# Optimization experiments

Hardware: AMD Instinct MI355X
Metric: run time of the kernel (lower is better)

The kernel has to match this reference:

```python
import jax, jax.numpy as jnp
import numpy as np

B_SZ, L_SEQ, ENC_IN = 8, 1024, 32
D_MODEL, D_INNER, D_STATE, D_CONV, DT_RANK = 256, 512, 16, 4, 16
N_LAYERS, D_FF, C_OUT = 2, 1024, 1


def setup_inputs() -> dict:
    key = jax.random.key(0)
    ks = jax.random.split(key, 16)
    s = 0.02
    inp = {}
    inp["x"] = jax.random.normal(ks[0], (B_SZ, L_SEQ, ENC_IN), jnp.float32)
    inp["in_w"] = jax.random.normal(ks[1], (D_MODEL, ENC_IN), jnp.float32) * s
    inp["in_b"] = jnp.zeros((D_MODEL,), jnp.float32)
    inp["in_proj_w"] = jax.random.normal(ks[2], (N_LAYERS, 2 * D_INNER, D_MODEL), jnp.float32) * s
    inp["conv_w"] = jax.random.normal(ks[3], (N_LAYERS, D_INNER, D_CONV), jnp.float32) * 0.1
    inp["conv_b"] = jnp.zeros((N_LAYERS, D_INNER), jnp.float32)
    inp["x_proj_w"] = jax.random.normal(ks[4], (N_LAYERS, DT_RANK + 2 * D_STATE, D_INNER), jnp.float32) * s
    inp["dt_w"] = jax.random.normal(ks[5], (N_LAYERS, D_INNER, DT_RANK), jnp.float32) * (DT_RANK ** -0.5)
    dt = jax.random.uniform(ks[6], (N_LAYERS, D_INNER), jnp.float32, 1e-3, 0.1)
    inp["dt_b"] = dt + jnp.log(-jnp.expm1(-dt))  # inverse softplus
    inp["A_log"] = jnp.tile(jnp.log(jnp.arange(1, D_STATE + 1, dtype=jnp.float32)), (N_LAYERS, D_INNER, 1))
    inp["D_skip"] = jnp.ones((N_LAYERS, D_INNER), jnp.float32)
    inp["out_proj_w"] = jax.random.normal(ks[7], (N_LAYERS, D_MODEL, D_INNER), jnp.float32) * s
    inp["p1_w"] = jax.random.normal(ks[8], (D_FF, D_MODEL), jnp.float32) * s
    inp["p1_b"] = jnp.zeros((D_FF,), jnp.float32)
    inp["p2_w"] = jax.random.normal(ks[9], (C_OUT, D_FF), jnp.float32) * s
    inp["p2_b"] = jnp.zeros((C_OUT,), jnp.float32)
    return inp


def causal_dw_conv(x, w, b):
    # x: [b, l, d], w: [d, k] depthwise, left-pad for causality
    xc = jax.lax.conv_general_dilated(
        x.transpose(0, 2, 1), w[:, None, :], (1,), [(D_CONV - 1, 0)],
        feature_group_count=D_INNER, dimension_numbers=("NCH", "OIH", "NCH"))
    return (xc + b[None, :, None]).transpose(0, 2, 1)


def selective_scan(u, dt, A, Bm, Cm):
    # u, dt: [b, l, d]; Bm, Cm: [b, l, n]; A: [d, n]
    def step(h, inp):
        u_t, dt_t, B_t, C_t = inp  # [b,d],[b,d],[b,n],[b,n]
        dA = jnp.exp(dt_t[..., None] * A)                      # [b,d,n]
        dBu = dt_t[..., None] * B_t[:, None, :] * u_t[..., None]
        h = dA * h + dBu
        y = jnp.einsum("bdn,bn->bd", h, C_t)
        return h, y
    h0 = jnp.zeros((u.shape[0], D_INNER, D_STATE), u.dtype)
    xs = (u.transpose(1, 0, 2), dt.transpose(1, 0, 2),
          Bm.transpose(1, 0, 2), Cm.transpose(1, 0, 2))
    _, ys = jax.lax.scan(step, h0, xs)
    return ys.transpose(1, 0, 2)  # [b, l, d]


def mamba_block(h, ipw, cw, cb, xpw, dtw, dtb, Alog, Dp, opw):
    xz = jnp.einsum("bld,ed->ble", h, ipw)          # [b,l,2*d_inner]
    xi, z = jnp.split(xz, 2, axis=-1)
    xc = jax.nn.silu(causal_dw_conv(xi, cw, cb))     # [b,l,d_inner]
    xdbl = jnp.einsum("bld,ed->ble", xc, xpw)        # [b,l,dt_rank+2n]
    dt_lo = xdbl[..., :DT_RANK]
    Bm = xdbl[..., DT_RANK:DT_RANK + D_STATE]
    Cm = xdbl[..., DT_RANK + D_STATE:]
    dt = jax.nn.softplus(jnp.einsum("blr,dr->bld", dt_lo, dtw) + dtb)
    A = -jnp.exp(Alog)
    y = selective_scan(xc, dt, A, Bm, Cm) + xc * Dp
    y = y * jax.nn.silu(z)
    return jnp.einsum("bld,ed->ble", y, opw)


def reference(x, in_w, in_b, in_proj_w, conv_w, conv_b, x_proj_w, dt_w, dt_b,
              A_log, D_skip, out_proj_w, p1_w, p1_b, p2_w, p2_b):
    h = jnp.einsum("bli,di->bld", x, in_w) + in_b
    for i in range(N_LAYERS):
        h = mamba_block(h, in_proj_w[i], conv_w[i], conv_b[i], x_proj_w[i],
                        dt_w[i], dt_b[i], A_log[i], D_skip[i], out_proj_w[i])
    h = h[:, -1, :]  # last timestep
    h = jax.nn.gelu(jnp.einsum("bd,fd->bf", h, p1_w) + p1_b, approximate=False)
    return jnp.einsum("bf,cf->bc", h, p2_w) + p2_b
```

## Files before the change

### kernel.cpp

```cpp
#include <hip/hip_runtime.h>
#include <math.h>


static constexpr int L_SEQ = 1024;
static constexpr int M_ROWS = 8 * 1024;
static constexpr int NCHUNK = 32;
static constexpr int TCHUNK = 32;

typedef unsigned short u16;
typedef unsigned short u16x8 __attribute__((ext_vector_type(8)));
typedef unsigned short u16x4 __attribute__((ext_vector_type(4)));
typedef short bf16x8 __attribute__((ext_vector_type(8)));
typedef float f32x4 __attribute__((ext_vector_type(4)));

__device__ __forceinline__ float silu_f(float x) { return x / (1.f + __expf(-x)); }
__device__ __forceinline__ float softplus_f(float x) {
  return (x > 20.f) ? x : log1pf(__expf(x));
}
__device__ __forceinline__ u16 f2bf(float f) {
  unsigned u = __builtin_bit_cast(unsigned, f);
  u += 0x7FFFu + ((u >> 16) & 1u);
  return (u16)(u >> 16);
}
__device__ __forceinline__ float bf2f(u16 v) {
  return __builtin_bit_cast(float, (unsigned)v << 16);
}

__device__ __forceinline__ void gll16(const u16* g, u16* l) {
  __builtin_amdgcn_global_load_lds(
      (const __attribute__((address_space(1))) void*)g,
      (__attribute__((address_space(3))) void*)l, 16, 0, 0);
}

template<int BM,int BN,int EPI,int OUTBF>
__global__ __launch_bounds__(256)
void gemm_db(const u16* __restrict__ A, int lda,
             const u16* __restrict__ W, int ldw,
             const float* __restrict__ bias,
             void* __restrict__ Cp, int ldc,
             int N, int K)
{
  constexpr int RWA = BM / 64, RWB = BN / 64;
  constexpr int NWA = 4 * RWA, NWB = 4 * RWB;
  constexpr int NWT = NWA + NWB;
  constexpr int TI = BM / 2 / 16;
  constexpr int TJ = BN / 2 / 16;

  __shared__ u16 As[2][BM * 32];
  __shared__ u16 Ws[2][BN * 32];

  const int tid = threadIdx.x;
  const int lane = tid & 63;
  const int wv = tid >> 6;
  const int wy = wv >> 1, wx = wv & 1;
  const int rb = wy * (BM / 2);
  const int cb = wx * (BN / 2);
  const int lr = lane & 15, lq = lane >> 4;
  const int bm = blockIdx.x * BM;
  const int bn = blockIdx.y * BN;

  f32x4 acc[TI][TJ];
#pragma unroll
  for (int i = 0; i < TI; ++i)
#pragma unroll
    for (int j = 0; j < TJ; ++j) acc[i][j] = (f32x4){0.f, 0.f, 0.f, 0.f};

  auto stage = [&](int k0, int buf) {
#pragma unroll
    for (int w = wv; w < NWT; w += 4) {
      if (w < NWA) {
        const int lqw = w / RWA, rh = w % RWA;
        gll16(A + (size_t)(bm + rh * 64 + lane) * lda + k0 + lqw * 8,
              &As[buf][(lqw * BM + rh * 64) * 8]);
      } else {
        const int w2 = w - NWA;
        const int lqw = w2 / RWB, rh = w2 % RWB;
        gll16(W + (size_t)(bn + rh * 64 + lane) * ldw + k0 + lqw * 8,
              &Ws[buf][(lqw * BN + rh * 64) * 8]);
      }
    }
  };

  stage(0, 0);
  int cur = 0;
  for (int k0 = 0; k0 < K; k0 += 32) {
    __syncthreads();
    if (k0 + 32 < K) stage(k0 + 32, cur ^ 1);

    bf16x8 af[TI], bf[TJ];
#pragma unroll
    for (int i = 0; i < TI; ++i)
      af[i] = *reinterpret_cast<const bf16x8*>(&As[cur][(lq * BM + rb + i * 16 + lr) * 8]);
#pragma unroll
    for (int j = 0; j < TJ; ++j)
      bf[j] = *reinterpret_cast<const bf16x8*>(&Ws[cur][(lq * BN + cb + j * 16 + lr) * 8]);
#pragma unroll
    for (int i = 0; i < TI; ++i)
#pragma unroll
      for (int j = 0; j < TJ; ++j)
        acc[i][j] = __builtin_amdgcn_mfma_f32_16x16x32_bf16(af[i], bf[j], acc[i][j], 0, 0, 0);
    cur ^= 1;
  }

#pragma unroll
  for (int i = 0; i < TI; ++i) {
#pragma unroll
    for (int j = 0; j < TJ; ++j) {
      const int col = bn + cb + j * 16 + lr;
      if (col >= N) continue;
#pragma unroll
      for (int r = 0; r < 4; ++r) {
        const int row = bm + rb + i * 16 + lq * 4 + r;
        float c = acc[i][j][r];
        if (EPI == 1) c += bias[col];
        if (EPI == 2) { if (col < 512) c = softplus_f(c + bias[col]); }
        if (OUTBF) ((u16*)Cp)[(size_t)row * ldc + col] = f2bf(c);
        else       ((float*)Cp)[(size_t)row * ldc + col] = c;
      }
    }
  }
}

__global__ __launch_bounds__(512)
void prep(const float* __restrict__ x, const float* __restrict__ in_w,
          const float* __restrict__ ipw, const float* __restrict__ opw,
          const float* __restrict__ dtw, const float* __restrict__ xpw,
          u16* __restrict__ x16, u16* __restrict__ inw16,
          u16* __restrict__ ipw16, u16* __restrict__ opw16,
          u16* __restrict__ wc)
{
  const int blk = blockIdx.x;
  if (blk < 516) {
    const float* src; u16* dst; int base;
    if (blk < 128)      { src = x;    dst = x16;   base = blk; }
    else if (blk < 132) { src = in_w; dst = inw16; base = blk - 128; }
    else if (blk < 388) { src = ipw;  dst = ipw16; base = blk - 132; }
    else                { src = opw;  dst = opw16; base = blk - 388; }
    const int i = (base * 512 + threadIdx.x) * 4;
    float4 v = *reinterpret_cast<const float4*>(src + i);
    u16x4 o;
    o[0] = f2bf(v.x); o[1] = f2bf(v.y); o[2] = f2bf(v.z); o[3] = f2bf(v.w);
    *reinterpret_cast<u16x4*>(dst + i) = o;
  } else {
    const int idx = blk - 516;
    const int layer = idx / 640;
    const int n = idx % 640;
    const int k = threadIdx.x;
    const float* xp = xpw + (size_t)layer * 48 * 512;
    float v = 0.f;
    if (n < 512) {
      const float* dw = dtw + (size_t)layer * 512 * 16 + n * 16;
#pragma unroll
      for (int r = 0; r < 16; ++r) v = fmaf(dw[r], xp[r * 512 + k], v);
    } else if (n < 544) {
      v = xp[(16 + (n - 512)) * 512 + k];
    }
    wc[((size_t)layer * 640 + n) * 512 + k] = f2bf(v);
  }
}

__global__ __launch_bounds__(512)
void conv_silu(const u16* __restrict__ xz, const float* __restrict__ cw,
               const float* __restrict__ cb, u16* __restrict__ xc)
{
  const int b = blockIdx.x;
  const int l0 = blockIdx.y * 32;
  const int d = threadIdx.x;

  const float w0 = cw[d * 4 + 0], w1 = cw[d * 4 + 1];
  const float w2 = cw[d * 4 + 2], w3 = cw[d * 4 + 3];
  const float bias = cb[d];

  const size_t base = ((size_t)b * L_SEQ) * 1024 + d;
  float xm3 = (l0 >= 3) ? bf2f(xz[base + (size_t)(l0 - 3) * 1024]) : 0.f;
  float xm2 = (l0 >= 2) ? bf2f(xz[base + (size_t)(l0 - 2) * 1024]) : 0.f;
  float xm1 = (l0 >= 1) ? bf2f(xz[base + (size_t)(l0 - 1) * 1024]) : 0.f;

#pragma unroll 4
  for (int i = 0; i < 32; ++i) {
    const int l = l0 + i;
    const float x0 = bf2f(xz[base + (size_t)l * 1024]);
    const float v = bias + w0 * xm3 + w1 * xm2 + w2 * xm1 + w3 * x0;
    xc[((size_t)b * L_SEQ + l) * 512 + d] = f2bf(silu_f(v));
    xm3 = xm2; xm2 = xm1; xm1 = x0;
  }
}

__global__ __launch_bounds__(256)
void scan_passA(const float* __restrict__ xo, const u16* __restrict__ u,
                const float* __restrict__ Alog,
                float* __restrict__ Ac, float* __restrict__ Bc)
{
  const int b = blockIdx.x;
  const int d = blockIdx.y * 256 + threadIdx.x;
  const int c = blockIdx.z;
  const int t0 = c * TCHUNK;

  __shared__ float sB[TCHUNK][16];
#pragma unroll
  for (int r = 0; r < TCHUNK * 16; r += 256) {
    const int e = threadIdx.x + r;
    const int t = e >> 4, n = e & 15;
    sB[t][n] = xo[((size_t)b * L_SEQ + t0 + t) * 544 + 512 + n];
  }
  __syncthreads();

  float A[16], h[16], p[16];
  const float* al = Alog + d * 16;
#pragma unroll
  for (int n = 0; n < 16; ++n) { A[n] = -__expf(al[n]); h[n] = 0.f; p[n] = 1.f; }

#pragma unroll 2
  for (int t = 0; t < TCHUNK; ++t) {
    const size_t row = (size_t)b * L_SEQ + t0 + t;
    const float dtv = xo[row * 544 + d];
    const float uv  = bf2f(u[row * 512 + d]);
    const float cf  = dtv * uv;
    const f32x4* Bq = reinterpret_cast<const f32x4*>(&sB[t][0]);
#pragma unroll
    for (int q = 0; q < 4; ++q) {
      const f32x4 Bv = Bq[q];
#pragma unroll
      for (int k = 0; k < 4; ++k) {
        const int n = q * 4 + k;
        const float dA = __expf(dtv * A[n]);
        p[n] *= dA;
        h[n] = fmaf(dA, h[n], cf * Bv[k]);
      }
    }
  }

  float* ac = Ac + (((size_t)b * NCHUNK + c) * 512 + d) * 16;
  float* bc = Bc + (((size_t)b * NCHUNK + c) * 512 + d) * 16;
#pragma unroll
  for (int q = 0; q < 4; ++q) {
    f32x4 va, vb;
#pragma unroll
    for (int k = 0; k < 4; ++k) { va[k] = p[q * 4 + k]; vb[k] = h[q * 4 + k]; }
    reinterpret_cast<f32x4*>(ac)[q] = va;
    reinterpret_cast<f32x4*>(bc)[q] = vb;
  }
}

__global__ __launch_bounds__(256)
void scan_mid(const float* __restrict__ Ac, const float* __restrict__ Bc,
              float* __restrict__ Hin)
{
  const int gid = blockIdx.x * 256 + threadIdx.x;
  const int b = gid >> 13;
  const int e = gid & 8191;
  float h = 0.f;
  for (int c = 0; c < NCHUNK; ++c) {
    const size_t idx = ((size_t)(b * NCHUNK + c)) * 8192 + e;
    Hin[idx] = h;
    h = fmaf(Ac[idx], h, Bc[idx]);
  }
}

__global__ __launch_bounds__(256)
void scan_passB(const float* __restrict__ xo, const u16* __restrict__ u,
                const u16* __restrict__ xz,
                const float* __restrict__ Alog, const float* __restrict__ Dsk,
                const float* __restrict__ Hin, u16* __restrict__ yg)
{
  const int b = blockIdx.x;
  const int d = blockIdx.y * 256 + threadIdx.x;
  const int c = blockIdx.z;
  const int t0 = c * TCHUNK;

  __shared__ float sB[TCHUNK][16], sC[TCHUNK][16];
#pragma unroll
  for (int r = 0; r < TCHUNK * 16; r += 256) {
    const int e = threadIdx.x + r;
    const int t = e >> 4, n = e & 15;
    const size_t row = (size_t)b * L_SEQ + t0 + t;
    sB[t][n] = xo[row * 544 + 512 + n];
    sC[t][n] = xo[row * 544 + 528 + n];
  }
  __syncthreads();

  float A[16], h[16];
  const float* al = Alog + d * 16;
#pragma unroll
  for (int n = 0; n < 16; ++n) A[n] = -__expf(al[n]);

  const float* hp = Hin + (((size_t)b * NCHUNK + c) * 512 + d) * 16;
#pragma unroll
  for (int q = 0; q < 4; ++q) {
    const f32x4 v = reinterpret_cast<const f32x4*>(hp)[q];
#pragma unroll
    for (int k = 0; k < 4; ++k) h[q * 4 + k] = v[k];
  }

  const float Dv = Dsk[d];

#pragma unroll 2
  for (int t = 0; t < TCHUNK; ++t) {
    const size_t row = (size_t)b * L_SEQ + t0 + t;
    const float dtv = xo[row * 544 + d];
    const float uv  = bf2f(u[row * 512 + d]);
    const float zf  = bf2f(xz[row * 1024 + 512 + d]);
    const float cf  = dtv * uv;
    const f32x4* Bq = reinterpret_cast<const f32x4*>(&sB[t][0]);
    const f32x4* Cq = reinterpret_cast<const f32x4*>(&sC[t][0]);
    float s0 = 0.f, s1 = 0.f, s2 = 0.f, s3 = 0.f;
#pragma unroll
    for (int q = 0; q < 4; ++q) {
      const f32x4 Bv = Bq[q];
      const f32x4 Cv = Cq[q];
#pragma unroll
      for (int k = 0; k < 4; ++k) {
        const int n = q * 4 + k;
        const float dA = __expf(dtv * A[n]);
        h[n] = fmaf(dA, h[n], cf * Bv[k]);
      }
      s0 = fmaf(h[q * 4 + 0], Cv[0], s0);
      s1 = fmaf(h[q * 4 + 1], Cv[1], s1);
      s2 = fmaf(h[q * 4 + 2], Cv[2], s2);
      s3 = fmaf(h[q * 4 + 3], Cv[3], s3);
    }
    const float yv = fmaf(uv, Dv, (s0 + s1) + (s2 + s3));
    yg[row * 512 + d] = f2bf(yv * silu_f(zf));
  }
}

__global__ __launch_bounds__(1024)
void head(const u16* __restrict__ h, const float* __restrict__ p1w,
          const float* __restrict__ p1b, const float* __restrict__ p2w,
          const float* __restrict__ p2b, float* __restrict__ out)
{
  const int b = blockIdx.x;
  const int f = threadIdx.x;

  __shared__ float hl[256];
  if (f < 256) hl[f] = bf2f(h[((size_t)b * L_SEQ + (L_SEQ - 1)) * 256 + f]);
  __syncthreads();

  const float* wr = p1w + (size_t)f * 256;
  float acc = 0.f;
#pragma unroll 8
  for (int k = 0; k < 256; k += 4) {
    float4 wv = *reinterpret_cast<const float4*>(wr + k);
    acc = fmaf(hl[k + 0], wv.x, acc);
    acc = fmaf(hl[k + 1], wv.y, acc);
    acc = fmaf(hl[k + 2], wv.z, acc);
    acc = fmaf(hl[k + 3], wv.w, acc);
  }
  const float xv = acc + p1b[f];
  const float gg = 0.5f * xv * (1.f + erff(xv * 0.70710678118654752f));
  float s = gg * p2w[f];

  s += __shfl_xor(s, 1);
  s += __shfl_xor(s, 2);
  s += __shfl_xor(s, 4);
  s += __shfl_xor(s, 8);
  s += __shfl_xor(s, 16);
  s += __shfl_xor(s, 32);
  __shared__ float red[16];
  if ((f & 63) == 0) red[f >> 6] = s;
  __syncthreads();
  if (f == 0) {
    float t = 0.f;
#pragma unroll
    for (int i = 0; i < 16; ++i) t += red[i];
    out[b] = t + p2b[0];
  }
}

extern "C" void kernel_launch(void* const* d_in, const int* in_sizes, int n_in,
                              void* d_out, int out_size, void* d_ws, size_t ws_size,
                              hipStream_t stream)
{
  const float* x    = (const float*)d_in[0];
  const float* in_w = (const float*)d_in[1];
  const float* in_b = (const float*)d_in[2];
  const float* ipw  = (const float*)d_in[3];
  const float* cw   = (const float*)d_in[4];
  const float* cb   = (const float*)d_in[5];
  const float* xpw  = (const float*)d_in[6];
  const float* dtw  = (const float*)d_in[7];
  const float* dtb  = (const float*)d_in[8];
  const float* Alog = (const float*)d_in[9];
  const float* Dsk  = (const float*)d_in[10];
  const float* opw  = (const float*)d_in[11];
  const float* p1w  = (const float*)d_in[12];
  const float* p1b  = (const float*)d_in[13];
  const float* p2w  = (const float*)d_in[14];
  const float* p2b  = (const float*)d_in[15];

  float* ws = (float*)d_ws;
  u16*   h16  = (u16*)(ws);
  u16*   xz16 = (u16*)(ws + 1048576);
  u16*   xc16 = (u16*)(ws + 5242880);
  float* xo   = ws + 7340032;
  u16*   wc16 = (u16*)(ws + 11796480);
  u16*   wbf  = (u16*)(ws + 12124160);
  float* Ac   = ws + 12660736;
  float* Bc   = ws + 14757888;
  float* Hin  = ws + 16855040;

  u16* x16   = wbf;
  u16* inw16 = wbf + 262144;
  u16* ipw16 = wbf + 270336;
  u16* opw16 = wbf + 794624;

  prep<<<1796, 512, 0, stream>>>(x, in_w, ipw, opw, dtw, xpw,
                                 x16, inw16, ipw16, opw16, wc16);

  gemm_db<64, 128, 1, 1><<<dim3(M_ROWS / 64, 2), 256, 0, stream>>>(
      x16, 32, inw16, 32, in_b, h16, 256, 256, 32);

  for (int layer = 0; layer < 2; ++layer) {
    const float* cw_l  = cw  + (size_t)layer * 512 * 4;
    const float* cb_l  = cb  + (size_t)layer * 512;
    const float* dtb_l = dtb + (size_t)layer * 512;
    const float* Al_l  = Alog + (size_t)layer * 512 * 16;
    const float* Dsk_l = Dsk + (size_t)layer * 512;
    const u16*   ipw_l = ipw16 + (size_t)layer * 1024 * 256;
    const u16*   opw_l = opw16 + (size_t)layer * 256 * 512;
    const u16*   wc_l  = wc16 + (size_t)layer * 640 * 512;

    gemm_db<64, 128, 0, 1><<<dim3(M_ROWS / 64, 8), 256, 0, stream>>>(
        h16, 256, ipw_l, 256, nullptr, xz16, 1024, 1024, 256);

    conv_silu<<<dim3(8, 32), 512, 0, stream>>>(xz16, cw_l, cb_l, xc16);

    gemm_db<64, 128, 2, 0><<<dim3(M_ROWS / 64, 5), 256, 0, stream>>>(
        xc16, 512, wc_l, 512, dtb_l, xo, 544, 544, 512);

    scan_passA<<<dim3(8, 2, NCHUNK), 256, 0, stream>>>(
        xo, xc16, Al_l, Ac, Bc);
    scan_mid<<<256, 256, 0, stream>>>(Ac, Bc, Hin);
    scan_passB<<<dim3(8, 2, NCHUNK), 256, 0, stream>>>(
        xo, xc16, xz16, Al_l, Dsk_l, Hin, xc16);

    gemm_db<64, 64, 0, 1><<<dim3(M_ROWS / 64, 4), 256, 0, stream>>>(
        xc16, 512, opw_l, 512, nullptr, h16, 256, 256, 512);
  }

  head<<<8, 1024, 0, stream>>>(h16, p1w, p1b, p2w, p2b, (float*)d_out);
}
```

Measured before the change: 374.1 us.

## Fold input projection into layer-0 in_proj, fuse scan_mid, widen GEMM K tile

Precomputes the product of the layer-0 in_proj weight and the input embedding weight, plus its bias, so the first two GEMMs collapse into one K=32 GEMM. The chunk-carry scan kernel is merged into scan_passA through an atomic last-block counter, so the last arriving block per (batch, d-half) computes the chunk prefix states. The GEMM gains a BK template parameter, set to 64 for the larger-K GEMMs, which halves the number of sync iterations. This removes two launches per layer and the h16 round trip, but the last-block tail is serial and the weight folding now runs in prep on every call.

```diff
diff --git a/kernel.cpp b/kernel.cpp
--- a/kernel.cpp
+++ b/kernel.cpp
@@ -32,7 +32,7 @@
       (__attribute__((address_space(3))) void*)l, 16, 0, 0);
 }
 
-template<int BM,int BN,int EPI,int OUTBF>
+template<int BM,int BN,int BK,int EPI,int OUTBF>
 __global__ __launch_bounds__(256)
 void gemm_db(const u16* __restrict__ A, int lda,
              const u16* __restrict__ W, int ldw,
@@ -40,14 +40,15 @@
              void* __restrict__ Cp, int ldc,
              int N, int K)
 {
-  constexpr int RWA = BM / 64, RWB = BN / 64;
-  constexpr int NWA = 4 * RWA, NWB = 4 * RWB;
-  constexpr int NWT = NWA + NWB;
+  constexpr int KS = BK / 32;
+  constexpr int CA = BK / 8;
+  constexpr int NCH_A = (BM / 64) * CA;
+  constexpr int NCH_B = (BN / 64) * CA;
   constexpr int TI = BM / 2 / 16;
   constexpr int TJ = BN / 2 / 16;
 
-  __shared__ u16 As[2][BM * 32];
-  __shared__ u16 Ws[2][BN * 32];
+  __shared__ u16 As[2][BM * BK];
+  __shared__ u16 Ws[2][BN * BK];
 
   const int tid = threadIdx.x;
   const int lane = tid & 63;
@@ -67,14 +68,14 @@
 
   auto stage = [&](int k0, int buf) {
 #pragma unroll
-    for (int w = wv; w < NWT; w += 4) {
-      if (w < NWA) {
-        const int lqw = w / RWA, rh = w % RWA;
+    for (int w = wv; w < NCH_A + NCH_B; w += 4) {
+      if (w < NCH_A) {
+        const int rh = w / CA, lqw = w % CA;
         gll16(A + (size_t)(bm + rh * 64 + lane) * lda + k0 + lqw * 8,
               &As[buf][(lqw * BM + rh * 64) * 8]);
       } else {
-        const int w2 = w - NWA;
-        const int lqw = w2 / RWB, rh = w2 % RWB;
+        const int w2 = w - NCH_A;
+        const int rh = w2 / CA, lqw = w2 % CA;
         gll16(W + (size_t)(bn + rh * 64 + lane) * ldw + k0 + lqw * 8,
               &Ws[buf][(lqw * BN + rh * 64) * 8]);
       }
@@ -83,22 +84,28 @@
 
   stage(0, 0);
   int cur = 0;
-  for (int k0 = 0; k0 < K; k0 += 32) {
+  for (int k0 = 0; k0 < K; k0 += BK) {
     __syncthreads();
-    if (k0 + 32 < K) stage(k0 + 32, cur ^ 1);
-
-    bf16x8 af[TI], bf[TJ];
-#pragma unroll
-    for (int i = 0; i < TI; ++i)
-      af[i] = *reinterpret_cast<const bf16x8*>(&As[cur][(lq * BM + rb + i * 16 + lr) * 8]);
-#pragma unroll
-    for (int j = 0; j < TJ; ++j)
-      bf[j] = *reinterpret_cast<const bf16x8*>(&Ws[cur][(lq * BN + cb + j * 16 + lr) * 8]);
-#pragma unroll
-    for (int i = 0; i < TI; ++i)
+    if (k0 + BK < K) stage(k0 + BK, cur ^ 1);
+
+#pragma unroll
+    for (int ks = 0; ks < KS; ++ks) {
+      const int lqc = ks * 4 + lq;
+      bf16x8 af[TI], bf[TJ];
+#pragma unroll
+      for (int i = 0; i < TI; ++i)
+        af[i] = *reinterpret_cast<const bf16x8*>(
+                  &As[cur][(lqc * BM + rb + i * 16 + lr) * 8]);
 #pragma unroll
       for (int j = 0; j < TJ; ++j)
-        acc[i][j] = __builtin_amdgcn_mfma_f32_16x16x32_bf16(af[i], bf[j], acc[i][j], 0, 0, 0);
+        bf[j] = *reinterpret_cast<const bf16x8*>(
+                  &Ws[cur][(lqc * BN + cb + j * 16 + lr) * 8]);
+#pragma unroll
+      for (int i = 0; i < TI; ++i)
+#pragma unroll
+        for (int j = 0; j < TJ; ++j)
+          acc[i][j] = __builtin_amdgcn_mfma_f32_16x16x32_bf16(af[i], bf[j], acc[i][j], 0, 0, 0);
+    }
     cur ^= 1;
   }
 
@@ -123,26 +130,40 @@
 
 __global__ __launch_bounds__(512)
 void prep(const float* __restrict__ x, const float* __restrict__ in_w,
+          const float* __restrict__ in_b,
           const float* __restrict__ ipw, const float* __restrict__ opw,
           const float* __restrict__ dtw, const float* __restrict__ xpw,
-          u16* __restrict__ x16, u16* __restrict__ inw16,
-          u16* __restrict__ ipw16, u16* __restrict__ opw16,
-          u16* __restrict__ wc)
+          u16* __restrict__ x16, u16* __restrict__ opw16,
+          u16* __restrict__ ipw16l1, u16* __restrict__ wc1,
+          float* __restrict__ bias1, u16* __restrict__ wc)
 {
   const int blk = blockIdx.x;
-  if (blk < 516) {
+  if (blk < 384) {
     const float* src; u16* dst; int base;
-    if (blk < 128)      { src = x;    dst = x16;   base = blk; }
-    else if (blk < 132) { src = in_w; dst = inw16; base = blk - 128; }
-    else if (blk < 388) { src = ipw;  dst = ipw16; base = blk - 132; }
-    else                { src = opw;  dst = opw16; base = blk - 388; }
+    if (blk < 128)      { src = x;            dst = x16;     base = blk; }
+    else if (blk < 256) { src = opw;          dst = opw16;   base = blk - 128; }
+    else                { src = ipw + 262144; dst = ipw16l1; base = blk - 256; }
     const int i = (base * 512 + threadIdx.x) * 4;
     float4 v = *reinterpret_cast<const float4*>(src + i);
     u16x4 o;
     o[0] = f2bf(v.x); o[1] = f2bf(v.y); o[2] = f2bf(v.z); o[3] = f2bf(v.w);
     *reinterpret_cast<u16x4*>(dst + i) = o;
+  } else if (blk < 448) {
+    const int t = threadIdx.x;
+    const int n = (blk - 384) * 16 + (t >> 5);
+    const int enc = t & 31;
+    const float* iprow = ipw + (size_t)n * 256;
+    float v = 0.f;
+#pragma unroll 8
+    for (int j = 0; j < 256; ++j) v = fmaf(iprow[j], in_w[j * 32 + enc], v);
+    wc1[n * 32 + enc] = f2bf(v);
+    if (enc == 0) {
+      float bv = 0.f;
+      for (int j = 0; j < 256; ++j) bv = fmaf(iprow[j], in_b[j], bv);
+      bias1[n] = bv;
+    }
   } else {
-    const int idx = blk - 516;
+    const int idx = blk - 448;
     const int layer = idx / 640;
     const int n = idx % 640;
     const int k = threadIdx.x;
@@ -189,7 +210,8 @@
 __global__ __launch_bounds__(256)
 void scan_passA(const float* __restrict__ xo, const u16* __restrict__ u,
                 const float* __restrict__ Alog,
-                float* __restrict__ Ac, float* __restrict__ Bc)
+                float* __restrict__ Ac, float* __restrict__ Bc,
+                float* __restrict__ Hin, unsigned* __restrict__ cnt)
 {
   const int b = blockIdx.x;
   const int d = blockIdx.y * 256 + threadIdx.x;
@@ -240,20 +262,35 @@
     reinterpret_cast<f32x4*>(ac)[q] = va;
     reinterpret_cast<f32x4*>(bc)[q] = vb;
   }
-}
-
-__global__ __launch_bounds__(256)
-void scan_mid(const float* __restrict__ Ac, const float* __restrict__ Bc,
-              float* __restrict__ Hin)
-{
-  const int gid = blockIdx.x * 256 + threadIdx.x;
-  const int b = gid >> 13;
-  const int e = gid & 8191;
-  float h = 0.f;
-  for (int c = 0; c < NCHUNK; ++c) {
-    const size_t idx = ((size_t)(b * NCHUNK + c)) * 8192 + e;
-    Hin[idx] = h;
-    h = fmaf(Ac[idx], h, Bc[idx]);
+
+  __syncthreads();
+  __shared__ unsigned lastf;
+  if (threadIdx.x == 0) {
+    __threadfence();
+    unsigned old = atomicAdd(&cnt[b * 2 + blockIdx.y], 1u);
+    lastf = (old == NCHUNK - 1) ? 1u : 0u;
+  }
+  __syncthreads();
+  if (lastf) {
+    __threadfence();
+    float hh[16];
+#pragma unroll
+    for (int n = 0; n < 16; ++n) hh[n] = 0.f;
+    for (int cc = 0; cc < NCHUNK; ++cc) {
+      const size_t base2 = (((size_t)b * NCHUNK + cc) * 512 + d) * 16;
+#pragma unroll
+      for (int q = 0; q < 4; ++q) {
+        const f32x4 va = reinterpret_cast<const f32x4*>(Ac + base2)[q];
+        const f32x4 vb = reinterpret_cast<const f32x4*>(Bc + base2)[q];
+        f32x4 ho;
+#pragma unroll
+        for (int k = 0; k < 4; ++k) {
+          ho[k] = hh[q * 4 + k];
+          hh[q * 4 + k] = fmaf(va[k], hh[q * 4 + k], vb[k]);
+        }
+        reinterpret_cast<f32x4*>(Hin + base2)[q] = ho;
+      }
+    }
   }
 }
 
@@ -398,45 +435,70 @@
   float* Ac   = ws + 12660736;
   float* Bc   = ws + 14757888;
   float* Hin  = ws + 16855040;
-
-  u16* x16   = wbf;
-  u16* inw16 = wbf + 262144;
-  u16* ipw16 = wbf + 270336;
-  u16* opw16 = wbf + 794624;
-
-  prep<<<1796, 512, 0, stream>>>(x, in_w, ipw, opw, dtw, xpw,
-                                 x16, inw16, ipw16, opw16, wc16);
-
-  gemm_db<64, 128, 1, 1><<<dim3(M_ROWS / 64, 2), 256, 0, stream>>>(
-      x16, 32, inw16, 32, in_b, h16, 256, 256, 32);
-
-  for (int layer = 0; layer < 2; ++layer) {
-    const float* cw_l  = cw  + (size_t)layer * 512 * 4;
-    const float* cb_l  = cb  + (size_t)layer * 512;
-    const float* dtb_l = dtb + (size_t)layer * 512;
-    const float* Al_l  = Alog + (size_t)layer * 512 * 16;
-    const float* Dsk_l = Dsk + (size_t)layer * 512;
-    const u16*   ipw_l = ipw16 + (size_t)layer * 1024 * 256;
-    const u16*   opw_l = opw16 + (size_t)layer * 256 * 512;
-    const u16*   wc_l  = wc16 + (size_t)layer * 640 * 512;
-
-    gemm_db<64, 128, 0, 1><<<dim3(M_ROWS / 64, 8), 256, 0, stream>>>(
-        h16, 256, ipw_l, 256, nullptr, xz16, 1024, 1024, 256);
+  u16*   wc1  = (u16*)(ws + 18952192);
+  float* bias1 = ws + 18968576;
+  unsigned* cnt = (unsigned*)(ws + 18969600);
+
+  u16* x16     = wbf;
+  u16* opw16   = wbf + 262144;
+  u16* ipw16l1 = wbf + 524288;
+
+  hipMemsetAsync(cnt, 0, 32 * sizeof(unsigned), stream);
+
+  prep<<<1728, 512, 0, stream>>>(x, in_w, in_b, ipw, opw, dtw, xpw,
+                                 x16, opw16, ipw16l1, wc1, bias1, wc16);
+
+  {
+    const float* cw_l  = cw;
+    const float* cb_l  = cb;
+    const float* dtb_l = dtb;
+    const float* Al_l  = Alog;
+    const float* Dsk_l = Dsk;
+    const u16*   opw_l = opw16;
+    const u16*   wc_l  = wc16;
+
+    gemm_db<64, 128, 32, 1, 1><<<dim3(M_ROWS / 64, 8), 256, 0, stream>>>(
+        x16, 32, wc1, 32, bias1, xz16, 1024, 1024, 32);
 
     conv_silu<<<dim3(8, 32), 512, 0, stream>>>(xz16, cw_l, cb_l, xc16);
 
-    gemm_db<64, 128, 2, 0><<<dim3(M_ROWS / 64, 5), 256, 0, stream>>>(
+    gemm_db<64, 128, 64, 2, 0><<<dim3(M_ROWS / 64, 5), 256, 0, stream>>>(
         xc16, 512, wc_l, 512, dtb_l, xo, 544, 544, 512);
 
     scan_passA<<<dim3(8, 2, NCHUNK), 256, 0, stream>>>(
-        xo, xc16, Al_l, Ac, Bc);
-    scan_mid<<<256, 256, 0, stream>>>(Ac, Bc, Hin);
+        xo, xc16, Al_l, Ac, Bc, Hin, cnt);
     scan_passB<<<dim3(8, 2, NCHUNK), 256, 0, stream>>>(
         xo, xc16, xz16, Al_l, Dsk_l, Hin, xc16);
 
-    gemm_db<64, 64, 0, 1><<<dim3(M_ROWS / 64, 4), 256, 0, stream>>>(
+    gemm_db<64, 64, 64, 0, 1><<<dim3(M_ROWS / 64, 4), 256, 0, stream>>>(
         xc16, 512, opw_l, 512, nullptr, h16, 256, 256, 512);
   }
 
+  {
+    const float* cw_l  = cw  + 512 * 4;
+    const float* cb_l  = cb  + 512;
+    const float* dtb_l = dtb + 512;
+    const float* Al_l  = Alog + 512 * 16;
+    const float* Dsk_l = Dsk + 512;
+    const u16*   opw_l = opw16 + 256 * 512;
+    const u16*   wc_l  = wc16 + 640 * 512;
+
+    gemm_db<64, 128, 64, 0, 1><<<dim3(M_ROWS / 64, 8), 256, 0, stream>>>(
+        h16, 256, ipw16l1, 256, nullptr, xz16, 1024, 1024, 256);
+
+    conv_silu<<<dim3(8, 32), 512, 0, stream>>>(xz16, cw_l, cb_l, xc16);
+
+    gemm_db<64, 128, 64, 2, 0><<<dim3(M_ROWS / 64, 5), 256, 0, stream>>>(
+        xc16, 512, wc_l, 512, dtb_l, xo, 544, 544, 512);
+
+    scan_passA<<<dim3(8, 2, NCHUNK), 256, 0, stream>>>(
+        xo, xc16, Al_l, Ac, Bc, Hin, cnt + 16);
+    scan_passB<<<dim3(8, 2, NCHUNK), 256, 0, stream>>>(
+        xo, xc16, xz16, Al_l, Dsk_l, Hin, xc16);
+
+    gemm_db<64, 64, 64, 0, 1><<<dim3(M_ROWS / 64, 4), 256, 0, stream>>>(
+        xc16, 512, opw_l, 512, nullptr, h16, 256, 256, 512);
+  }
+
   head<<<8, 1024, 0, stream>>>(h16, p1w, p1b, p2w, p2b, (float*)d_out);
 }
```

After: 467.6 us. +25.0%, slower.
